# Kernel optimization log

Hardware: AMD Instinct MI355X
Metric: run time of the kernel (lower is better)

Reference implementation:

```python
import jax, jax.numpy as jnp
import numpy as np

C = 256      # n_embd
H = 16       # n_head
HS = C // H  # head_size = 16
B = 64
T = 256      # <= block_size
LN_EPS = 1e-5


def _layer_norm(x, g, b):
    mu = jnp.mean(x, axis=-1, keepdims=True)
    var = jnp.mean((x - mu) ** 2, axis=-1, keepdims=True)
    return (x - mu) * jax.lax.rsqrt(var + LN_EPS) * g + b


def setup_inputs() -> dict:
    key = jax.random.key(0)
    ks = jax.random.split(key, 10)
    s_in = 1.0 / np.sqrt(C)
    s_ff = 1.0 / np.sqrt(4 * C)
    return {
        "x": jax.random.normal(ks[0], (B, T, C), dtype=jnp.float32),
        # per-head Q/K/V weights, stacked: [H, C, HS] (no bias, as in Head)
        "Wq": jax.random.normal(ks[1], (H, C, HS), dtype=jnp.float32) * s_in,
        "Wk": jax.random.normal(ks[2], (H, C, HS), dtype=jnp.float32) * s_in,
        "Wv": jax.random.normal(ks[3], (H, C, HS), dtype=jnp.float32) * s_in,
        "Wp": jax.random.normal(ks[4], (C, C), dtype=jnp.float32) * s_in,
        "bp": jnp.zeros((C,), dtype=jnp.float32),
        "W1": jax.random.normal(ks[5], (C, 4 * C), dtype=jnp.float32) * s_in,
        "b1": jnp.zeros((4 * C,), dtype=jnp.float32),
        "W2": jax.random.normal(ks[6], (4 * C, C), dtype=jnp.float32) * s_ff,
        "b2": jnp.zeros((C,), dtype=jnp.float32),
        "g1": jnp.ones((C,), dtype=jnp.float32),
        "be1": jnp.zeros((C,), dtype=jnp.float32),
        "g2": jnp.ones((C,), dtype=jnp.float32),
        "be2": jnp.zeros((C,), dtype=jnp.float32),
    }


def reference(x, Wq, Wk, Wv, Wp, bp, W1, b1, W2, b2, g1, be1, g2, be2):
    Bx, Tx, Cx = x.shape
    h = _layer_norm(x, g1, be1)
    # per-head projections: [B, H, T, HS]
    q = jnp.einsum('btc,hcd->bhtd', h, Wq)
    k = jnp.einsum('btc,hcd->bhtd', h, Wk)
    v = jnp.einsum('btc,hcd->bhtd', h, Wv)
    # NOTE: original scales by C**-0.5 with C = n_embd, NOT head_size
    scale = 1.0 / np.sqrt(Cx)
    scores = jnp.einsum('bhtd,bhsd->bhts', q, k) * scale
    causal = jnp.tril(jnp.ones((Tx, Tx), dtype=bool))
    scores = jnp.where(causal, scores, -jnp.inf)
    wei = jax.nn.softmax(scores, axis=-1)  # dropout = identity (eval)
    attn = jnp.einsum('bhts,bhsd->bhtd', wei, v)
    # concat heads in order -> [B, T, C]
    attn = attn.transpose(0, 2, 1, 3).reshape(Bx, Tx, Cx)
    attn = attn @ Wp + bp
    x = x + attn
    h2 = _layer_norm(x, g2, be2)
    ffn = jax.nn.gelu(h2 @ W1 + b1, approximate=False) @ W2 + b2
    return x + ffn


if __name__ == "__main__":
    out = reference(**setup_inputs())
    print(out.shape, out.dtype)
```

## Files before the change

kernel.cpp:

```cpp
#include <hip/hip_runtime.h>
#include <hip/hip_bf16.h>

typedef __attribute__((ext_vector_type(8))) short short8;
typedef __attribute__((ext_vector_type(4))) float f32x4;
typedef __attribute__((ext_vector_type(16))) float f32x16;

__device__ __forceinline__ unsigned short f2bf(float f) {
    unsigned u = __float_as_uint(f);
    unsigned r = (u + 0x7fffu + ((u >> 16) & 1u)) >> 16;
    return (unsigned short)r;
}
__device__ __forceinline__ float bf2f(unsigned short h) {
    return __uint_as_float(((unsigned)h) << 16);
}

__device__ __forceinline__ float fast_gelu(float v) {
    float y  = 0.7978845608f * v * (1.0f + 0.044715f * v * v);
    float ay = fabsf(y);
    float e  = __expf(2.0f * ay);
    float th = 1.0f - 2.0f / (e + 1.0f);
    th = __builtin_copysignf(th, y);
    return 0.5f * v * (1.0f + th);
}

__device__ __forceinline__ void gload16(const unsigned short* g, unsigned short* l) {
    __builtin_amdgcn_global_load_lds(
        (const __attribute__((address_space(1))) unsigned int*)g,
        (__attribute__((address_space(3))) unsigned int*)l,
        16, 0, 0);
}

template<int N> __device__ __forceinline__ void vmwait() {
    asm volatile("s_waitcnt vmcnt(%0)" :: "n"(N) : "memory");
}
__device__ __forceinline__ void barrier_raw() {
    asm volatile("" ::: "memory");
    __builtin_amdgcn_s_barrier();
    asm volatile("" ::: "memory");
}

__global__ __launch_bounds__(256) void prep_ln1(
    const float* __restrict__ Wq, const float* __restrict__ Wk,
    const float* __restrict__ Wv, const float* __restrict__ Wp,
    const float* __restrict__ W1, const float* __restrict__ W2,
    unsigned short* __restrict__ WqkvT, unsigned short* __restrict__ WpT,
    unsigned short* __restrict__ W1T, unsigned short* __restrict__ W2T,
    const float* __restrict__ xin, const float* __restrict__ gw,
    const float* __restrict__ bw, unsigned short* __restrict__ h1)
{
    __shared__ float smem[4096];
    const int bid = blockIdx.x, t = threadIdx.x;
    if (bid >= 624) {
        int row  = (bid - 624) * 4 + (t >> 6);
        int lane = t & 63;
        const float4 v = *reinterpret_cast<const float4*>(xin + (size_t)row * 256 + lane * 4);
        float s  = v.x + v.y + v.z + v.w;
        float sq = v.x*v.x + v.y*v.y + v.z*v.z + v.w*v.w;
#pragma unroll
        for (int m = 1; m < 64; m <<= 1) { s += __shfl_xor(s, m); sq += __shfl_xor(sq, m); }
        float mean = s * (1.0f/256.0f);
        float var  = sq * (1.0f/256.0f) - mean*mean;
        float rstd = rsqrtf(var + 1e-5f);
        const float4 g4 = *reinterpret_cast<const float4*>(gw + lane*4);
        const float4 b4 = *reinterpret_cast<const float4*>(bw + lane*4);
        ushort4 o;
        o.x = f2bf((v.x-mean)*rstd*g4.x + b4.x);
        o.y = f2bf((v.y-mean)*rstd*g4.y + b4.y);
        o.z = f2bf((v.z-mean)*rstd*g4.z + b4.z);
        o.w = f2bf((v.w-mean)*rstd*g4.w + b4.w);
        *reinterpret_cast<ushort4*>(h1 + (size_t)row*256 + lane*4) = o;
        return;
    }
    if (bid < 576) {
        const float* W; unsigned short* WT; int N, K, tile0;
        if (bid < 64)       { W = Wp; WT = WpT; N = 256;  K = 256;  tile0 = bid; }
        else if (bid < 320) { W = W1; WT = W1T; N = 1024; K = 256;  tile0 = bid - 64; }
        else                { W = W2; WT = W2T; N = 256;  K = 1024; tile0 = bid - 320; }
        int ntx = N >> 5;
        int bx = tile0 % ntx, by = tile0 / ntx;
        int c0 = bx*32, r0 = by*32;
        int tx = t & 31, ty = t >> 5;
#pragma unroll
        for (int i = 0; i < 4; ++i)
            smem[(ty + i*8)*33 + tx] = W[(size_t)(r0 + ty + i*8)*N + c0 + tx];
        __syncthreads();
#pragma unroll
        for (int i = 0; i < 4; ++i)
            WT[(size_t)(c0 + ty + i*8)*K + r0 + tx] = f2bf(smem[tx*33 + ty + i*8]);
    } else {
        int pb = bid - 576;
        int proj = pb >> 4, hh = pb & 15;
        const float* W = (proj == 0) ? Wq : ((proj == 1) ? Wk : Wv);
        float scale = (proj == 0) ? 0.0625f : 1.0f;
        const float4* src = reinterpret_cast<const float4*>(W + hh*4096);
#pragma unroll
        for (int i = 0; i < 4; ++i) {
            float4 v4 = src[t + i*256];
            *reinterpret_cast<float4*>(&smem[(t + i*256)*4]) = v4;
        }
        __syncthreads();
        int d = t >> 4, cp = (t & 15) * 16;
        unsigned short obuf[16];
#pragma unroll
        for (int i = 0; i < 16; ++i)
            obuf[i] = f2bf(smem[(cp + i)*16 + d] * scale);
        unsigned short* dst = WqkvT + (size_t)(proj*256 + hh*16 + d)*256 + cp;
        *reinterpret_cast<ushort4*>(dst)      = *reinterpret_cast<ushort4*>(&obuf[0]);
        *reinterpret_cast<ushort4*>(dst + 4)  = *reinterpret_cast<ushort4*>(&obuf[4]);
        *reinterpret_cast<ushort4*>(dst + 8)  = *reinterpret_cast<ushort4*>(&obuf[8]);
        *reinterpret_cast<ushort4*>(dst + 12) = *reinterpret_cast<ushort4*>(&obuf[12]);
    }
}

template<int NBX>
__device__ __forceinline__ void swz_bid(int& bx, int& by) {
    int nwg = gridDim.x;
    int bid = blockIdx.x;
    int vid = (bid & 7) * (nwg >> 3) + (bid >> 3);
    bx = vid % NBX;
    by = vid / NBX;
}

template<int BM, int BN, int K>
__device__ __forceinline__ void gemm_core(
    const unsigned short* __restrict__ A, const unsigned short* __restrict__ BT,
    int bx, int by, f32x4 (&acc)[BM/32][BN/32])
{
    constexpr int FM = BM/32, FN = BN/32, NT = K/32;
    constexpr int LA = BM/64, LB = BN/64, L = LA + LB;
    __shared__ unsigned short As[3][BM*32];
    __shared__ unsigned short Bs[3][BN*32];
    const int tid = threadIdx.x, lane = tid & 63, wid = tid >> 6;
    const int wr = (wid >> 1) * (BM/2), wc = (wid & 1) * (BN/2);
    const int c16 = lane & 15, g16 = lane >> 4;
    const int lr = lane >> 2, lq = lane & 3;

#pragma unroll
    for (int m = 0; m < FM; ++m)
#pragma unroll
        for (int n = 0; n < FN; ++n) acc[m][n] = f32x4{0.f, 0.f, 0.f, 0.f};

    const unsigned short* a0 = A  + (size_t)(by*BM + lr)*K + lq*8;
    const unsigned short* b0 = BT + (size_t)(bx*BN + lr)*K + lq*8;

    auto stage = [&](int buf, int t) {
        int k0 = t * 32;
#pragma unroll
        for (int i = 0; i < LA; ++i) {
            int ch = wid*LA + i;
            gload16(a0 + (size_t)ch*16*K + k0, &As[buf][ch*512]);
        }
#pragma unroll
        for (int i = 0; i < LB; ++i) {
            int ch = wid*LB + i;
            gload16(b0 + (size_t)ch*16*K + k0, &Bs[buf][ch*512]);
        }
    };

    auto compute = [&](int buf) {
        short8 af[FM], bf[FN];
#pragma unroll
        for (int m = 0; m < FM; ++m)
            af[m] = *reinterpret_cast<const short8*>(&As[buf][(wr + m*16 + c16)*32 + g16*8]);
#pragma unroll
        for (int n = 0; n < FN; ++n)
            bf[n] = *reinterpret_cast<const short8*>(&Bs[buf][(wc + n*16 + c16)*32 + g16*8]);
#pragma unroll
        for (int m = 0; m < FM; ++m)
#pragma unroll
            for (int n = 0; n < FN; ++n)
                acc[m][n] = __builtin_amdgcn_mfma_f32_16x16x32_bf16(af[m], bf[n], acc[m][n], 0, 0, 0);
    };

    stage(0, 0);
    stage(1, 1);
    int cur = 0;
    for (int t = 0; t < NT; ++t) {
        vmwait<L>();
        barrier_raw();
        if (t + 2 < NT) {
            int nb = cur + 2; if (nb >= 3) nb -= 3;
            stage(nb, t + 2);
        }
        compute(cur);
        ++cur; if (cur == 3) cur = 0;
    }
}

template<int BM, int BN, int K>
__device__ __forceinline__ void gemm_core8(
    const unsigned short* __restrict__ A, const unsigned short* __restrict__ BT,
    int bx, int by, f32x4 (&acc)[BM/32][BN/64])
{
    constexpr int FM = BM/32, FN = BN/64, NT = K/32;
    constexpr int NCHA = BM/16, NCH = BM/16 + BN/16;
    constexpr int NR = (NCH + 7) / 8;
    constexpr int NFULL = NCH / 8, NREM = NCH % 8;
    __shared__ unsigned short As[3][BM*32];
    __shared__ unsigned short Bs[3][BN*32];
    const int tid = threadIdx.x, lane = tid & 63, wid = tid >> 6;
    const int wm = wid >> 2, wn = wid & 3;
    const int c16 = lane & 15, g16 = lane >> 4;
    const int lr = lane >> 2, lq = lane & 3;

#pragma unroll
    for (int m = 0; m < FM; ++m)
#pragma unroll
        for (int n = 0; n < FN; ++n) acc[m][n] = f32x4{0.f, 0.f, 0.f, 0.f};

    const unsigned short* a0 = A  + (size_t)(by*BM + lr)*K + lq*8;
    const unsigned short* b0 = BT + (size_t)(bx*BN + lr)*K + lq*8;

    auto stage = [&](int buf, int t) {
        int k0 = t * 32;
#pragma unroll
        for (int i = 0; i < NR; ++i) {
            int ch = i*8 + wid;
            if (ch < NCHA)
                gload16(a0 + (size_t)ch*16*K + k0, &As[buf][ch*512]);
            else if (ch < NCH)
                gload16(b0 + (size_t)(ch-NCHA)*16*K + k0, &Bs[buf][(ch-NCHA)*512]);
        }
    };

    auto compute = [&](int buf) {
        short8 af[FM], bf[FN];
#pragma unroll
        for (int m = 0; m < FM; ++m)
            af[m] = *reinterpret_cast<const short8*>(&As[buf][(wm*(BM/2) + m*16 + c16)*32 + g16*8]);
#pragma unroll
        for (int n = 0; n < FN; ++n)
            bf[n] = *reinterpret_cast<const short8*>(&Bs[buf][(wn*(BN/4) + n*16 + c16)*32 + g16*8]);
#pragma unroll
        for (int m = 0; m < FM; ++m)
#pragma unroll
            for (int n = 0; n < FN; ++n)
                acc[m][n] = __builtin_amdgcn_mfma_f32_16x16x32_bf16(af[m], bf[n], acc[m][n], 0, 0, 0);
    };

    stage(0, 0);
    stage(1, 1);
    int cur = 0;
    for (int t = 0; t < NT; ++t) {
        if constexpr (NREM == 0) {
            vmwait<NFULL>();
        } else {
            if (wid < NREM) vmwait<NFULL + 1>();
            else            vmwait<NFULL>();
        }
        barrier_raw();
        if (t + 2 < NT) {
            int nb = cur + 2; if (nb >= 3) nb -= 3;
            stage(nb, t + 2);
        }
        compute(cur);
        ++cur; if (cur == 3) cur = 0;
    }
}

__global__ __launch_bounds__(256) void gemm_qkv(
    const unsigned short* __restrict__ A, const unsigned short* __restrict__ BT,
    unsigned short* __restrict__ qb, unsigned short* __restrict__ kb,
    unsigned short* __restrict__ vtb)
{
    int bx, by; swz_bid<6>(bx, by);
    f32x4 acc[4][4];
    gemm_core<128, 128, 256>(A, BT, bx, by, acc);
    const int lane = threadIdx.x & 63, wid = threadIdx.x >> 6;
    const int c16 = lane & 15, g16 = lane >> 4;
    const int wr = (wid >> 1) * 64, wc = (wid & 1) * 64;
#pragma unroll
    for (int m = 0; m < 4; ++m)
#pragma unroll
    for (int n = 0; n < 4; ++n)
#pragma unroll
    for (int j = 0; j < 4; ++j) {
        int row = by*128 + wr + m*16 + g16*4 + j;
        int col = bx*128 + wc + n*16 + c16;
        int proj = col >> 8, hh = (col >> 4) & 15, dd = col & 15;
        int b = row >> 8, t = row & 255;
        unsigned short val = f2bf(acc[m][n][j]);
        size_t bh = (size_t)(b*16 + hh);
        if (proj == 0)      qb[(bh*256 + t)*16 + dd] = val;
        else if (proj == 1) kb[(bh*256 + t)*16 + dd] = val;
        else                vtb[(bh*16 + dd)*256 + t] = val;
    }
}

__global__ __launch_bounds__(512) void gemm_wp_ln(
    const unsigned short* __restrict__ A, const unsigned short* __restrict__ BT,
    const float* __restrict__ bp, const float* __restrict__ x,
    const float* __restrict__ g2, const float* __restrict__ be2,
    unsigned short* __restrict__ x2b, unsigned short* __restrict__ h2)
{
    int bx, by; swz_bid<1>(bx, by);
    f32x4 acc[2][4];
    gemm_core8<64, 256, 256>(A, BT, 0, by, acc);

    __shared__ float rs[64][4];
    __shared__ float rq[64][4];
    const int tid = threadIdx.x, lane = tid & 63, wid = tid >> 6;
    const int c16 = lane & 15, g16 = lane >> 4;
    const int wm = wid >> 2, wn = wid & 3;

    float vv[2][4][4];
#pragma unroll
    for (int m = 0; m < 2; ++m)
#pragma unroll
    for (int n = 0; n < 4; ++n)
#pragma unroll
    for (int j = 0; j < 4; ++j) {
        int row = by*64 + wm*32 + m*16 + g16*4 + j;
        int col = wn*64 + n*16 + c16;
        size_t idx = (size_t)row*256 + col;
        float v = acc[m][n][j] + bp[col] + x[idx];
        vv[m][n][j] = v;
        x2b[idx] = f2bf(v);
    }
#pragma unroll
    for (int m = 0; m < 2; ++m)
#pragma unroll
    for (int j = 0; j < 4; ++j) {
        float ps = vv[m][0][j] + vv[m][1][j] + vv[m][2][j] + vv[m][3][j];
        float pq = vv[m][0][j]*vv[m][0][j] + vv[m][1][j]*vv[m][1][j]
                 + vv[m][2][j]*vv[m][2][j] + vv[m][3][j]*vv[m][3][j];
#pragma unroll
        for (int mask = 1; mask < 16; mask <<= 1) {
            ps += __shfl_xor(ps, mask);
            pq += __shfl_xor(pq, mask);
        }
        if (c16 == 0) {
            int r = wm*32 + m*16 + g16*4 + j;
            rs[r][wn] = ps;
            rq[r][wn] = pq;
        }
    }
    __syncthreads();
#pragma unroll
    for (int m = 0; m < 2; ++m)
#pragma unroll
    for (int j = 0; j < 4; ++j) {
        int r = wm*32 + m*16 + g16*4 + j;
        float s = rs[r][0] + rs[r][1] + rs[r][2] + rs[r][3];
        float q = rq[r][0] + rq[r][1] + rq[r][2] + rq[r][3];
        float mean = s * (1.0f/256.0f);
        float var  = q * (1.0f/256.0f) - mean*mean;
        float rstd = rsqrtf(var + 1e-5f);
        int row = by*64 + r;
#pragma unroll
        for (int n = 0; n < 4; ++n) {
            int col = wn*64 + n*16 + c16;
            h2[(size_t)row*256 + col] = f2bf((vv[m][n][j]-mean)*rstd*g2[col] + be2[col]);
        }
    }
}

__global__ __launch_bounds__(512) void gemm_ffn1(
    const unsigned short* __restrict__ A, const unsigned short* __restrict__ BT,
    const float* __restrict__ b1, unsigned short* __restrict__ ffh)
{
    int bx, by; swz_bid<4>(bx, by);
    f32x4 acc[4][4];
    gemm_core8<128, 256, 256>(A, BT, bx, by, acc);
    const int lane = threadIdx.x & 63, wid = threadIdx.x >> 6;
    const int c16 = lane & 15, g16 = lane >> 4;
    const int wm = wid >> 2, wn = wid & 3;
#pragma unroll
    for (int m = 0; m < 4; ++m)
#pragma unroll
    for (int n = 0; n < 4; ++n)
#pragma unroll
    for (int j = 0; j < 4; ++j) {
        int row = by*128 + wm*64 + m*16 + g16*4 + j;
        int col = bx*256 + wn*64 + n*16 + c16;
        float v = acc[m][n][j] + b1[col];
        ffh[(size_t)row*1024 + col] = f2bf(fast_gelu(v));
    }
}

__global__ __launch_bounds__(512) void gemm_ffn2(
    const unsigned short* __restrict__ A, const unsigned short* __restrict__ BT,
    const float* __restrict__ b2, const unsigned short* __restrict__ x2b,
    float* __restrict__ out)
{
    int bx, by; swz_bid<1>(bx, by);
    f32x4 acc[2][4];
    gemm_core8<64, 256, 1024>(A, BT, 0, by, acc);
    const int lane = threadIdx.x & 63, wid = threadIdx.x >> 6;
    const int c16 = lane & 15, g16 = lane >> 4;
    const int wm = wid >> 2, wn = wid & 3;
#pragma unroll
    for (int m = 0; m < 2; ++m)
#pragma unroll
    for (int n = 0; n < 4; ++n)
#pragma unroll
    for (int j = 0; j < 4; ++j) {
        int row = by*64 + wm*32 + m*16 + g16*4 + j;
        int col = wn*64 + n*16 + c16;
        size_t idx = (size_t)row*256 + col;
        out[idx] = acc[m][n][j] + b2[col] + bf2f(x2b[idx]);
    }
}

__global__ __launch_bounds__(256) void attn_kernel(
    const unsigned short* __restrict__ qb, const unsigned short* __restrict__ kb,
    const unsigned short* __restrict__ vtb, unsigned short* __restrict__ ao)
{
    const int bid  = blockIdx.x;
    const int half = bid & 1, h = (bid >> 1) & 15, b = bid >> 5;
    const int tid  = threadIdx.x;
    const int w    = tid >> 6, lane = tid & 63;
    const int l31  = lane & 31, hi = lane >> 5;
    const int chunk = half*4 + w;
    const int t0    = chunk * 32;
    const unsigned short* qh = qb  + (size_t)(b*16 + h) * 4096;
    const unsigned short* kh = kb  + (size_t)(b*16 + h) * 4096;
    const unsigned short* vh = vtb + (size_t)(b*16 + h) * 4096;

    short8 qf = *reinterpret_cast<const short8*>(qh + (size_t)(t0 + l31)*16 + hi*8);

    f32x16 zf, pv;
#pragma unroll
    for (int i = 0; i < 16; ++i) { zf[i] = 0.f; pv[i] = 0.f; }
    float sum = 0.f;
    const int dref = l31 & 15;

    for (int tt = 0; tt <= chunk; ++tt) {
        short8 kf = *reinterpret_cast<const short8*>(kh + (size_t)(tt*32 + l31)*16 + hi*8);
        f32x16 S = __builtin_amdgcn_mfma_f32_32x32x16_bf16(kf, qf, zf, 0, 0, 0);

        float p[16];
#pragma unroll
        for (int r = 0; r < 16; ++r) {
            float pe = __expf(S[r]);
            if (tt == chunk) {
                int s_local = (r & 3) + 8*(r >> 2) + 4*hi;
                pe = (s_local <= l31) ? pe : 0.f;
            }
            p[r] = pe;
            sum += pe;
        }

        unsigned qd[8], xd[8];
#pragma unroll
        for (int i = 0; i < 8; ++i) {
            unsigned rr;
            asm("v_cvt_pk_bf16_f32 %0, %1, %2" : "=v"(rr) : "v"(p[2*i]), "v"(p[2*i+1]));
            qd[i] = rr;
        }
#pragma unroll
        for (int i = 0; i < 8; ++i) xd[i] = (unsigned)__shfl_xor((int)qd[i], 32);

        int4 flo, fhi;
        flo.x = hi ? (int)xd[2] : (int)qd[0];
        flo.y = hi ? (int)xd[3] : (int)qd[1];
        flo.z = hi ? (int)qd[2] : (int)xd[0];
        flo.w = hi ? (int)qd[3] : (int)xd[1];
        fhi.x = hi ? (int)xd[6] : (int)qd[4];
        fhi.y = hi ? (int)xd[7] : (int)qd[5];
        fhi.z = hi ? (int)qd[6] : (int)xd[4];
        fhi.w = hi ? (int)qd[7] : (int)xd[5];
        short8 plo = __builtin_bit_cast(short8, flo);
        short8 phi = __builtin_bit_cast(short8, fhi);

        short8 vf0 = *reinterpret_cast<const short8*>(vh + (size_t)dref*256 + tt*32 + hi*8);
        short8 vf1 = *reinterpret_cast<const short8*>(vh + (size_t)dref*256 + tt*32 + 16 + hi*8);
        pv = __builtin_amdgcn_mfma_f32_32x32x16_bf16(vf0, plo, pv, 0, 0, 0);
        pv = __builtin_amdgcn_mfma_f32_32x32x16_bf16(vf1, phi, pv, 0, 0, 0);
    }

    sum += __shfl_xor(sum, 32);
    float rinv = 1.0f / sum;

    unsigned o0, o1, o2, o3;
    {
        float a0 = pv[0]*rinv, a1 = pv[1]*rinv, a2 = pv[2]*rinv, a3 = pv[3]*rinv;
        float a4 = pv[4]*rinv, a5 = pv[5]*rinv, a6 = pv[6]*rinv, a7 = pv[7]*rinv;
        asm("v_cvt_pk_bf16_f32 %0, %1, %2" : "=v"(o0) : "v"(a0), "v"(a1));
        asm("v_cvt_pk_bf16_f32 %0, %1, %2" : "=v"(o1) : "v"(a2), "v"(a3));
        asm("v_cvt_pk_bf16_f32 %0, %1, %2" : "=v"(o2) : "v"(a4), "v"(a5));
        asm("v_cvt_pk_bf16_f32 %0, %1, %2" : "=v"(o3) : "v"(a6), "v"(a7));
    }
    unsigned short* orow = ao + (size_t)(b*256 + t0 + l31)*256 + h*16;
    uint2 s01 = {o0, o1}, s23 = {o2, o3};
    *reinterpret_cast<uint2*>(orow + hi*4)     = s01;
    *reinterpret_cast<uint2*>(orow + 8 + hi*4) = s23;
}

extern "C" void kernel_launch(void* const* d_in, const int* in_sizes, int n_in,
                              void* d_out, int out_size, void* d_ws, size_t ws_size,
                              hipStream_t stream)
{
    const float* x   = (const float*)d_in[0];
    const float* Wq  = (const float*)d_in[1];
    const float* Wk  = (const float*)d_in[2];
    const float* Wv  = (const float*)d_in[3];
    const float* Wp  = (const float*)d_in[4];
    const float* bp  = (const float*)d_in[5];
    const float* W1  = (const float*)d_in[6];
    const float* b1  = (const float*)d_in[7];
    const float* W2  = (const float*)d_in[8];
    const float* b2  = (const float*)d_in[9];
    const float* g1  = (const float*)d_in[10];
    const float* be1 = (const float*)d_in[11];
    const float* g2  = (const float*)d_in[12];
    const float* be2 = (const float*)d_in[13];
    float* out = (float*)d_out;

    char* ws = (char*)d_ws;
    unsigned short* h1    = (unsigned short*)(ws);
    unsigned short* WqkvT = (unsigned short*)(ws +  8388608);
    unsigned short* WpT   = (unsigned short*)(ws +  8781824);
    unsigned short* W1T   = (unsigned short*)(ws +  8912896);
    unsigned short* W2T   = (unsigned short*)(ws +  9437184);
    unsigned short* qb    = (unsigned short*)(ws +  9961472);
    unsigned short* kb    = (unsigned short*)(ws + 18350080);
    unsigned short* vtb   = (unsigned short*)(ws + 26738688);
    unsigned short* ao    = (unsigned short*)(ws + 35127296);
    unsigned short* ffh   = qb;
    unsigned short* x2b   = (unsigned short*)(ws + 43515904);
    unsigned short* h2    = (unsigned short*)(ws + 60293120);

    prep_ln1<<<4720, 256, 0, stream>>>(Wq, Wk, Wv, Wp, W1, W2,
                                       WqkvT, WpT, W1T, W2T, x, g1, be1, h1);
    gemm_qkv<<<768, 256, 0, stream>>>(h1, WqkvT, qb, kb, vtb);
    attn_kernel<<<2048, 256, 0, stream>>>(qb, kb, vtb, ao);
    gemm_wp_ln<<<256, 512, 0, stream>>>(ao, WpT, bp, x, g2, be2, x2b, h2);
    gemm_ffn1<<<512, 512, 0, stream>>>(h2, W1T, b1, ffh);
    gemm_ffn2<<<256, 512, 0, stream>>>(ffh, W2T, b2, x2b, out);
}
```

Before: 109.2 us.

## Move QKV GEMM to 8-wave 128x256 tile core and peel last pipeline iteration

The QKV projection GEMM switches from the 4-wave 128x128 core to the 8-wave gemm_core8 with a 128x256 tile. This halves the grid to 384 blocks of 512 threads and raises B-operand reuse per block. The shared pipeline loop now peels its final iteration with a full vmcnt(0) wait, and its barrier now also waits for outstanding LDS reads (lgkmcnt(0)), which affects all GEMMs using gemm_core8. The risks are fewer blocks to fill the CUs and the extra LDS waits at each barrier.

New measurement: 116.6 us. 1.07x slower.

```diff
diff --git a/kernel.cpp b/kernel.cpp
--- a/kernel.cpp
+++ b/kernel.cpp
@@ -33,8 +33,8 @@
 template<int N> __device__ __forceinline__ void vmwait() {
     asm volatile("s_waitcnt vmcnt(%0)" :: "n"(N) : "memory");
 }
-__device__ __forceinline__ void barrier_raw() {
-    asm volatile("" ::: "memory");
+__device__ __forceinline__ void pipe_barrier() {
+    asm volatile("s_waitcnt lgkmcnt(0)" ::: "memory");
     __builtin_amdgcn_s_barrier();
     asm volatile("" ::: "memory");
 }
@@ -122,72 +122,6 @@
 }
 
 template<int BM, int BN, int K>
-__device__ __forceinline__ void gemm_core(
-    const unsigned short* __restrict__ A, const unsigned short* __restrict__ BT,
-    int bx, int by, f32x4 (&acc)[BM/32][BN/32])
-{
-    constexpr int FM = BM/32, FN = BN/32, NT = K/32;
-    constexpr int LA = BM/64, LB = BN/64, L = LA + LB;
-    __shared__ unsigned short As[3][BM*32];
-    __shared__ unsigned short Bs[3][BN*32];
-    const int tid = threadIdx.x, lane = tid & 63, wid = tid >> 6;
-    const int wr = (wid >> 1) * (BM/2), wc = (wid & 1) * (BN/2);
-    const int c16 = lane & 15, g16 = lane >> 4;
-    const int lr = lane >> 2, lq = lane & 3;
-
-#pragma unroll
-    for (int m = 0; m < FM; ++m)
-#pragma unroll
-        for (int n = 0; n < FN; ++n) acc[m][n] = f32x4{0.f, 0.f, 0.f, 0.f};
-
-    const unsigned short* a0 = A  + (size_t)(by*BM + lr)*K + lq*8;
-    const unsigned short* b0 = BT + (size_t)(bx*BN + lr)*K + lq*8;
-
-    auto stage = [&](int buf, int t) {
-        int k0 = t * 32;
-#pragma unroll
-        for (int i = 0; i < LA; ++i) {
-            int ch = wid*LA + i;
-            gload16(a0 + (size_t)ch*16*K + k0, &As[buf][ch*512]);
-        }
-#pragma unroll
-        for (int i = 0; i < LB; ++i) {
-            int ch = wid*LB + i;
-            gload16(b0 + (size_t)ch*16*K + k0, &Bs[buf][ch*512]);
-        }
-    };
-
-    auto compute = [&](int buf) {
-        short8 af[FM], bf[FN];
-#pragma unroll
-        for (int m = 0; m < FM; ++m)
-            af[m] = *reinterpret_cast<const short8*>(&As[buf][(wr + m*16 + c16)*32 + g16*8]);
-#pragma unroll
-        for (int n = 0; n < FN; ++n)
-            bf[n] = *reinterpret_cast<const short8*>(&Bs[buf][(wc + n*16 + c16)*32 + g16*8]);
-#pragma unroll
-        for (int m = 0; m < FM; ++m)
-#pragma unroll
-            for (int n = 0; n < FN; ++n)
-                acc[m][n] = __builtin_amdgcn_mfma_f32_16x16x32_bf16(af[m], bf[n], acc[m][n], 0, 0, 0);
-    };
-
-    stage(0, 0);
-    stage(1, 1);
-    int cur = 0;
-    for (int t = 0; t < NT; ++t) {
-        vmwait<L>();
-        barrier_raw();
-        if (t + 2 < NT) {
-            int nb = cur + 2; if (nb >= 3) nb -= 3;
-            stage(nb, t + 2);
-        }
-        compute(cur);
-        ++cur; if (cur == 3) cur = 0;
-    }
-}
-
-template<int BM, int BN, int K>
 __device__ __forceinline__ void gemm_core8(
     const unsigned short* __restrict__ A, const unsigned short* __restrict__ BT,
     int bx, int by, f32x4 (&acc)[BM/32][BN/64])
@@ -241,14 +175,14 @@
     stage(0, 0);
     stage(1, 1);
     int cur = 0;
-    for (int t = 0; t < NT; ++t) {
+    for (int t = 0; t < NT - 1; ++t) {
         if constexpr (NREM == 0) {
             vmwait<NFULL>();
         } else {
             if (wid < NREM) vmwait<NFULL + 1>();
             else            vmwait<NFULL>();
         }
-        barrier_raw();
+        pipe_barrier();
         if (t + 2 < NT) {
             int nb = cur + 2; if (nb >= 3) nb -= 3;
             stage(nb, t + 2);
@@ -256,27 +190,30 @@
         compute(cur);
         ++cur; if (cur == 3) cur = 0;
     }
-}
-
-__global__ __launch_bounds__(256) void gemm_qkv(
+    vmwait<0>();
+    pipe_barrier();
+    compute(cur);
+}
+
+__global__ __launch_bounds__(512) void gemm_qkv(
     const unsigned short* __restrict__ A, const unsigned short* __restrict__ BT,
     unsigned short* __restrict__ qb, unsigned short* __restrict__ kb,
     unsigned short* __restrict__ vtb)
 {
-    int bx, by; swz_bid<6>(bx, by);
+    int bx, by; swz_bid<3>(bx, by);
     f32x4 acc[4][4];
-    gemm_core<128, 128, 256>(A, BT, bx, by, acc);
+    gemm_core8<128, 256, 256>(A, BT, bx, by, acc);
     const int lane = threadIdx.x & 63, wid = threadIdx.x >> 6;
     const int c16 = lane & 15, g16 = lane >> 4;
-    const int wr = (wid >> 1) * 64, wc = (wid & 1) * 64;
+    const int wm = wid >> 2, wn = wid & 3;
 #pragma unroll
     for (int m = 0; m < 4; ++m)
 #pragma unroll
     for (int n = 0; n < 4; ++n)
 #pragma unroll
     for (int j = 0; j < 4; ++j) {
-        int row = by*128 + wr + m*16 + g16*4 + j;
-        int col = bx*128 + wc + n*16 + c16;
+        int row = by*128 + wm*64 + m*16 + g16*4 + j;
+        int col = bx*256 + wn*64 + n*16 + c16;
         int proj = col >> 8, hh = (col >> 4) & 15, dd = col & 15;
         int b = row >> 8, t = row & 255;
         unsigned short val = f2bf(acc[m][n][j]);
@@ -523,7 +460,7 @@
 
     prep_ln1<<<4720, 256, 0, stream>>>(Wq, Wk, Wv, Wp, W1, W2,
                                        WqkvT, WpT, W1T, W2T, x, g1, be1, h1);
-    gemm_qkv<<<768, 256, 0, stream>>>(h1, WqkvT, qb, kb, vtb);
+    gemm_qkv<<<384, 512, 0, stream>>>(h1, WqkvT, qb, kb, vtb);
     attn_kernel<<<2048, 256, 0, stream>>>(qb, kb, vtb, ao);
     gemm_wp_ln<<<256, 512, 0, stream>>>(ao, WpT, bp, x, g2, be2, x2b, h2);
     gemm_ffn1<<<512, 512, 0, stream>>>(h2, W1T, b1, ffh);
```
